# Optimization experiments

Measured on AMD Instinct MI355X. Metric: run time of the kernel, lower is better.

Reference implementation:

```python
import jax, jax.numpy as jnp
import numpy as np

N_NODES, N_EDGES, N_GRAPHS = 200000, 600000, 4000
IN_DIM, EDGE_DIM, HIDDEN, DEPTH = 25, 11, 128, 4
BN_EPS = 1e-5

def lrelu(x):
    return jnp.where(x > 0, x, 0.1 * x)

def setup_inputs() -> dict:
    key = jax.random.key(0)
    ks = jax.random.split(key, 8)
    x = jax.random.normal(ks[0], (N_NODES, IN_DIM), jnp.float32)
    edge_index = jax.random.randint(ks[1], (2, N_EDGES), 0, N_NODES, jnp.int32)
    edge_attr = jax.random.normal(ks[2], (N_EDGES, EDGE_DIM), jnp.float32)
    batch = jnp.sort(jax.random.randint(ks[3], (N_NODES,), 0, N_GRAPHS, jnp.int32))
    def init_w(k, shape, fan_in):
        return jax.random.normal(k, shape, jnp.float32) * np.float32(1.0 / np.sqrt(fan_in))
    W_in = init_w(ks[4], (IN_DIM, HIDDEN), IN_DIM)
    b_in = jnp.zeros((HIDDEN,), jnp.float32)
    W_msg = init_w(ks[5], (DEPTH, HIDDEN + EDGE_DIM, HIDDEN), HIDDEN + EDGE_DIM)
    b_msg = jnp.zeros((DEPTH, HIDDEN), jnp.float32)
    W_up = init_w(ks[6], (DEPTH, 2 * HIDDEN, HIDDEN), 2 * HIDDEN)
    b_up = jnp.zeros((DEPTH, HIDDEN), jnp.float32)
    gamma = jnp.ones((DEPTH, HIDDEN), jnp.float32)
    beta = jnp.zeros((DEPTH, HIDDEN), jnp.float32)
    return dict(x=x, edge_index=edge_index, edge_attr=edge_attr, batch=batch,
                W_in=W_in, b_in=b_in, W_msg=W_msg, b_msg=b_msg,
                W_up=W_up, b_up=b_up, gamma=gamma, beta=beta)

def reference(x, edge_index, edge_attr, batch, W_in, b_in, W_msg, b_msg, W_up, b_up, gamma, beta):
    N = x.shape[0]
    src, dst = edge_index[0], edge_index[1]  # PyG: x_j = x[src], aggregate at dst
    h = lrelu(x @ W_in + b_in)  # input_proj + leaky_relu(0.1)
    depth = W_msg.shape[0]
    for i in range(depth):
        # message: leaky_relu(Linear(cat[x_j, edge_attr]))
        msg = lrelu(jnp.concatenate([h[src], edge_attr], axis=-1) @ W_msg[i] + b_msg[i])
        aggr = jax.ops.segment_sum(msg, dst, num_segments=N)  # scatter-add
        # update: leaky_relu(Linear(cat[aggr, x]))
        out = lrelu(jnp.concatenate([aggr, h], axis=-1) @ W_up[i] + b_up[i])
        out = jax.nn.relu(out)
        # BatchNorm over node dim (training-mode batch statistics)
        mu = out.mean(axis=0)
        var = out.var(axis=0)
        h = gamma[i] * (out - mu) * jax.lax.rsqrt(var + BN_EPS) + beta[i]
        # dropout is identity at eval
    cnt = jax.ops.segment_sum(jnp.ones((N,), h.dtype), batch, num_segments=N_GRAPHS)
    summed = jax.ops.segment_sum(h, batch, num_segments=N_GRAPHS)
    return summed / jnp.maximum(cnt, 1.0)[:, None]  # global_mean_pool -> [G, H]
```

## Files before the change

kernel.cpp:

```cpp
#include <hip/hip_runtime.h>

#define N_NODES  200000
#define N_EDGES  600000
#define N_GRAPHS 4000
#define IN_DIM   25
#define EDGE_DIM 11
#define HIDDEN   128
#define DEPTH    4
#define BN_EPS   1e-5f

#define UB   32
#define NBLK (N_NODES / UB)
#define NEBLK (N_EDGES / 64)
#define CHUNK  256
#define NCHUNK ((N_NODES + CHUNK - 1) / CHUNK)

typedef unsigned short ushortT;
typedef __attribute__((ext_vector_type(8))) short short8v;
typedef __attribute__((ext_vector_type(4))) float float4v;

__device__ __forceinline__ float lrelu(float v) { return v > 0.f ? v : 0.1f * v; }

__device__ __forceinline__ ushortT f2bf(float f) {
    unsigned u = __builtin_bit_cast(unsigned, f);
    u = (u + 0x7fffu + ((u >> 16) & 1u)) >> 16;
    return (ushortT)u;
}
__device__ __forceinline__ float bf2f(ushortT h) {
    unsigned u = ((unsigned)h) << 16;
    return __builtin_bit_cast(float, u);
}

__global__ void k_hist(const int* __restrict__ ei, int* __restrict__ cnt)
{
    const int e = blockIdx.x * 256 + threadIdx.x;
    if (e < N_EDGES) atomicAdd(&cnt[ei[N_EDGES + e]], 1);
}

__global__ __launch_bounds__(256) void k_chunk_sum(const int* __restrict__ cnt,
                                                   int* __restrict__ bsum)
{
    const int t = threadIdx.x;
    const int i = blockIdx.x * CHUNK + t;
    int v = (i < N_NODES) ? cnt[i] : 0;
    #pragma unroll
    for (int off = 32; off > 0; off >>= 1) v += __shfl_down(v, off);
    __shared__ int ws[4];
    if ((t & 63) == 0) ws[t >> 6] = v;
    __syncthreads();
    if (t == 0) bsum[blockIdx.x] = ws[0] + ws[1] + ws[2] + ws[3];
}

__global__ __launch_bounds__(1024) void k_scan_bsums(const int* __restrict__ bsum,
                                                     int* __restrict__ bscan)
{
    __shared__ int s[1024];
    const int t = threadIdx.x;
    const int v = (t < NCHUNK) ? bsum[t] : 0;
    s[t] = v; __syncthreads();
    for (int off = 1; off < 1024; off <<= 1) {
        const int x = (t >= off) ? s[t - off] : 0;
        __syncthreads();
        s[t] += x;
        __syncthreads();
    }
    if (t < NCHUNK) bscan[t] = s[t] - v;
}

__global__ __launch_bounds__(256) void k_chunk_scan(const int* __restrict__ cnt,
                                                    const int* __restrict__ bscan,
                                                    int* __restrict__ off_work)
{
    __shared__ int s[CHUNK];
    const int b = blockIdx.x, t = threadIdx.x;
    const int i = b * CHUNK + t;
    const int v = (i < N_NODES) ? cnt[i] : 0;
    s[t] = v; __syncthreads();
    for (int off = 1; off < CHUNK; off <<= 1) {
        const int x = (t >= off) ? s[t - off] : 0;
        __syncthreads();
        s[t] += x;
        __syncthreads();
    }
    if (i < N_NODES) off_work[i] = bscan[b] + s[t] - v;
}

__global__ void k_scatter(const int* __restrict__ ei, int* __restrict__ off_work,
                          int* __restrict__ srcS, int* __restrict__ dstS,
                          int* __restrict__ perm)
{
    const int e = blockIdx.x * 256 + threadIdx.x;
    if (e < N_EDGES) {
        const int d = ei[N_EDGES + e];
        const int pos = atomicAdd(&off_work[d], 1);
        srcS[pos] = ei[e];
        dstS[pos] = d;
        perm[pos] = e;
    }
}

__global__ void k_flag_ends(const int* __restrict__ dstS, int* __restrict__ flag)
{
    const int i = blockIdx.x * 256 + threadIdx.x;
    if (i < NEBLK * 8) {
        const int b = i >> 3, p = i & 7;
        const int pp = (p >> 1) * 16 + ((p & 1) ? 15 : 0);
        flag[dstS[b * 64 + pp]] = 1;
    }
}

__global__ void k_flag_zdeg(const int* __restrict__ ecnt, int* __restrict__ flag)
{
    const int n = blockIdx.x * 256 + threadIdx.x;
    if (n < N_NODES && ecnt[n] == 0) flag[n] = 1;
}

__global__ void k_compact(const int* __restrict__ flag, int* __restrict__ zlist,
                          int* __restrict__ zcount)
{
    const int n = blockIdx.x * 256 + threadIdx.x;
    if (n < N_NODES && flag[n]) zlist[atomicAdd(zcount, 1)] = n;
}

__global__ __launch_bounds__(256) void k_zero_rows(const int* __restrict__ zlist,
                                                   const int* __restrict__ zcount,
                                                   float* __restrict__ aggr)
{
    const int total = zcount[0] * 32;
    const float4 z = {0.f, 0.f, 0.f, 0.f};
    for (int i = blockIdx.x * 256 + threadIdx.x; i < total; i += gridDim.x * 256) {
        const int row = zlist[i >> 5], q = i & 31;
        reinterpret_cast<float4*>(aggr)[(size_t)row * 32 + q] = z;
    }
}

__global__ __launch_bounds__(256) void k_prep_ea(const float* __restrict__ ea,
                                                 const int* __restrict__ perm,
                                                 ushortT* __restrict__ ea16)
{
    const size_t i = (size_t)blockIdx.x * 256 + threadIdx.x;
    if (i >= (size_t)N_EDGES * 16) return;
    const int e = (int)(i >> 4), c = (int)(i & 15);
    const int pe = perm[e];
    ea16[i] = (c < EDGE_DIM) ? f2bf(ea[(size_t)pe * EDGE_DIM + c]) : (ushortT)0;
}

__global__ __launch_bounds__(256) void k_fold(const float* __restrict__ Wm,
                                              const float* __restrict__ bm,
                                              const float* __restrict__ Wu,
                                              const float* __restrict__ bu,
                                              const float* __restrict__ scale,
                                              const float* __restrict__ shift,
                                              ushortT* __restrict__ WmF,
                                              float*   __restrict__ bmF,
                                              ushortT* __restrict__ WuF,
                                              float*   __restrict__ buF)
{
    const int b = blockIdx.x, t = threadIdx.x;
    if (b < 80) {
        const int i = b * 256 + t;
        const int j = i & 7, lane = (i >> 3) & 63, tile = i >> 9;
        const int ct = tile & 7, kt = tile >> 3;
        const int k = kt * 32 + ((lane >> 4) << 3) + j;
        const int c = ct * 16 + (lane & 15);
        float v = (k < HIDDEN + EDGE_DIM) ? Wm[k * HIDDEN + c] : 0.f;
        if (k < HIDDEN) v *= scale[k];
        WmF[i] = f2bf(v);
    } else if (b < 208) {
        const int i = (b - 80) * 256 + t;
        const int j = i & 7, lane = (i >> 3) & 63, tile = i >> 9;
        const int ct = tile & 7, kt = tile >> 3;
        const int k = kt * 32 + ((lane >> 4) << 3) + j;
        const int c = ct * 16 + (lane & 15);
        float v = Wu[k * HIDDEN + c];
        if (k >= HIDDEN) v *= scale[k - HIDDEN];
        WuF[i] = f2bf(v);
    } else if (b == 208) {
        if (t < HIDDEN) {
            float acc = bm[t];
            for (int k = 0; k < HIDDEN; ++k) acc += shift[k] * Wm[k * HIDDEN + t];
            bmF[t] = acc;
        }
    } else {
        if (t < HIDDEN) {
            float acc = bu[t];
            for (int k = 0; k < HIDDEN; ++k) acc += shift[k] * Wu[(HIDDEN + k) * HIDDEN + t];
            buF[t] = acc;
        }
    }
}

__global__ void k_init_affine(float* __restrict__ scale, float* __restrict__ shift)
{
    const int t = threadIdx.x;
    scale[t] = 1.f;
    shift[t] = 0.f;
}

__global__ __launch_bounds__(128) void k_input_proj(const float* __restrict__ x,
                                                    const float* __restrict__ W,
                                                    const float* __restrict__ b,
                                                    ushortT* __restrict__ h16)
{
    const int t  = threadIdx.x;
    const int n0 = blockIdx.x * 8;
    __shared__ float sW[IN_DIM * HIDDEN];
    __shared__ float sx[8][IN_DIM];
    for (int i = t; i < IN_DIM * HIDDEN; i += 128) sW[i] = W[i];
    for (int i = t; i < 8 * IN_DIM; i += 128) {
        int n = i / IN_DIM, k = i % IN_DIM;
        sx[n][k] = x[(size_t)(n0 + n) * IN_DIM + k];
    }
    __syncthreads();
    const float bt = b[t];
    for (int n = 0; n < 8; ++n) {
        float acc = bt;
        #pragma unroll
        for (int k = 0; k < IN_DIM; ++k) acc += sx[n][k] * sW[k * HIDDEN + t];
        h16[(size_t)(n0 + n) * HIDDEN + t] = f2bf(lrelu(acc));
    }
}

__global__ __launch_bounds__(256) void k_edge_mfma(const ushortT* __restrict__ h16,
                                                   const int*     __restrict__ srcS,
                                                   const int*     __restrict__ dstS,
                                                   const ushortT* __restrict__ ea16,
                                                   const ushortT* __restrict__ Wf,
                                                   const float*   __restrict__ bmsg,
                                                   float*         __restrict__ aggr)
{
    const int t    = threadIdx.x;
    const int wave = t >> 6, lane = t & 63;
    const int e0   = blockIdx.x * 64;

    __shared__ __align__(16) unsigned char smem[64 * 168 * 2];
    ushortT (*sA)[168]   = reinterpret_cast<ushortT (*)[168]>(smem);
    float   (*sMsg)[132] = reinterpret_cast<float (*)[132]>(smem);
    __shared__ int sSrc[64];
    __shared__ int sDst[64];

    const int ct0 = wave * 2;
    short8v B[5][2];
    const short8v* wp = reinterpret_cast<const short8v*>(Wf);
    #pragma unroll
    for (int kt = 0; kt < 5; ++kt) {
        B[kt][0] = wp[(size_t)(kt * 8 + ct0) * 64 + lane];
        B[kt][1] = wp[(size_t)(kt * 8 + ct0 + 1) * 64 + lane];
    }

    if (t < 64) { sSrc[t] = srcS[e0 + t]; sDst[t] = dstS[e0 + t]; }
    __syncthreads();

    for (int i = t; i < 64 * 16; i += 256) {
        const int e = i >> 4, q = i & 15;
        const uint4 v = reinterpret_cast<const uint4*>(h16)[(size_t)sSrc[e] * 16 + q];
        *reinterpret_cast<uint4*>(&sA[e][q * 8]) = v;
    }
    for (int i = t; i < 64 * 2; i += 256) {
        const int e = i >> 1, q = i & 1;
        const uint4 v = reinterpret_cast<const uint4*>(ea16)[((size_t)(e0 + e)) * 2 + q];
        *reinterpret_cast<uint4*>(&sA[e][128 + q * 8]) = v;
    }
    if (t < 128) {
        const int e = t >> 1, q = t & 1;
        const uint4 z = {0u, 0u, 0u, 0u};
        *reinterpret_cast<uint4*>(&sA[e][144 + q * 8]) = z;
    }
    __syncthreads();

    float4v acc[4][2];
    #pragma unroll
    for (int m = 0; m < 4; ++m) { acc[m][0] = (float4v)(0.f); acc[m][1] = (float4v)(0.f); }

    const int kOff = (lane >> 4) * 8;
    #pragma unroll
    for (int m = 0; m < 4; ++m) {
        const int row = m * 16 + (lane & 15);
        #pragma unroll
        for (int kt = 0; kt < 5; ++kt) {
            const short8v a = *reinterpret_cast<const short8v*>(&sA[row][kt * 32 + kOff]);
            acc[m][0] = __builtin_amdgcn_mfma_f32_16x16x32_bf16(a, B[kt][0], acc[m][0], 0, 0, 0);
            acc[m][1] = __builtin_amdgcn_mfma_f32_16x16x32_bf16(a, B[kt][1], acc[m][1], 0, 0, 0);
        }
    }
    __syncthreads();

    const int col = lane & 15;
    const int r0  = (lane >> 4) * 4;
    const int grp = t >> 7;
    const int c   = t & 127;

    #pragma unroll
    for (int phase = 0; phase < 2; ++phase) {
        #pragma unroll
        for (int mm = 0; mm < 2; ++mm) {
            const int m = phase * 2 + mm;
            #pragma unroll
            for (int cc = 0; cc < 2; ++cc) {
                const int ccol = (ct0 + cc) * 16 + col;
                const float bt = bmsg[ccol];
                #pragma unroll
                for (int j = 0; j < 4; ++j) {
                    sMsg[mm * 16 + r0 + j][ccol] = lrelu(acc[m][cc][j] + bt);
                }
            }
        }
        __syncthreads();
        const int base = phase * 32 + grp * 16;
        float a = 0.f;
        int cur = sDst[base];
        bool atStart = true;
        for (int i = 0; i < 16; ++i) {
            const int e = base + i;
            const int d = sDst[e];
            if (d != cur) {
                if (atStart) atomicAdd(&aggr[(size_t)cur * HIDDEN + c], a);
                else         aggr[(size_t)cur * HIDDEN + c] = a;
                atStart = false; cur = d; a = 0.f;
            }
            a += sMsg[e - phase * 32][c];
        }
        atomicAdd(&aggr[(size_t)cur * HIDDEN + c], a);
        __syncthreads();
    }
}

__global__ __launch_bounds__(512) void k_update_mfma(const float*   __restrict__ aggr,
                                                     const ushortT* __restrict__ h16,
                                                     const ushortT* __restrict__ Wf,
                                                     const float*   __restrict__ bup,
                                                     ushortT*       __restrict__ hout,
                                                     float*         __restrict__ p_sum,
                                                     float*         __restrict__ p_sumsq)
{
    const int t    = threadIdx.x;
    const int wave = t >> 6, lane = t & 63;
    const int n0   = blockIdx.x * UB;

    __shared__ __align__(16) ushortT sA[UB][264];
    __shared__ __align__(16) ushortT sLo[UB][136];

    const int ct = wave;
    short8v Bh[8];
    const short8v* wp = reinterpret_cast<const short8v*>(Wf);
    #pragma unroll
    for (int kt = 0; kt < 8; ++kt) Bh[kt] = wp[(size_t)(kt * 8 + ct) * 64 + lane];

    for (int i = t; i < UB * 32; i += 512) {
        const int n = i >> 5, q = i & 31;
        const float4 v = reinterpret_cast<const float4*>(aggr)[(size_t)(n0 + n) * 32 + q];
        union { ushortT s[4]; uint2 u; } hi, lo;
        #pragma unroll
        for (int j = 0; j < 4; ++j) {
            const float f = (&v.x)[j];
            const ushortT hb = f2bf(f);
            hi.s[j] = hb;
            lo.s[j] = f2bf(f - bf2f(hb));
        }
        *reinterpret_cast<uint2*>(&sA[n][q * 4])  = hi.u;
        *reinterpret_cast<uint2*>(&sLo[n][q * 4]) = lo.u;
    }
    for (int i = t; i < UB * 16; i += 512) {
        const int n = i >> 4, q = i & 15;
        const uint4 v = reinterpret_cast<const uint4*>(h16)[(size_t)(n0 + n) * 16 + q];
        *reinterpret_cast<uint4*>(&sA[n][128 + q * 8]) = v;
    }
    __syncthreads();

    float4v acc[2];
    acc[0] = (float4v)(0.f); acc[1] = (float4v)(0.f);

    const int kOff = (lane >> 4) * 8;
    #pragma unroll
    for (int m = 0; m < 2; ++m) {
        const int row = m * 16 + (lane & 15);
        #pragma unroll
        for (int kt = 0; kt < 8; ++kt) {
            const short8v a = *reinterpret_cast<const short8v*>(&sA[row][kt * 32 + kOff]);
            acc[m] = __builtin_amdgcn_mfma_f32_16x16x32_bf16(a, Bh[kt], acc[m], 0, 0, 0);
        }
        #pragma unroll
        for (int kt = 0; kt < 4; ++kt) {
            const short8v a = *reinterpret_cast<const short8v*>(&sLo[row][kt * 32 + kOff]);
            acc[m] = __builtin_amdgcn_mfma_f32_16x16x32_bf16(a, Bh[kt], acc[m], 0, 0, 0);
        }
    }

    const int col  = lane & 15;
    const int r0   = (lane >> 4) * 4;
    const int ccol = ct * 16 + col;
    const float bt = bup[ccol];
    float s = 0.f, q = 0.f;
    #pragma unroll
    for (int m = 0; m < 2; ++m) {
        #pragma unroll
        for (int j = 0; j < 4; ++j) {
            const float v = fmaxf(acc[m][j] + bt, 0.f);
            s += v; q += v * v;
            hout[(size_t)(n0 + m * 16 + r0 + j) * HIDDEN + ccol] = f2bf(v);
        }
    }
    s += __shfl_xor(s, 16); s += __shfl_xor(s, 32);
    q += __shfl_xor(q, 16); q += __shfl_xor(q, 32);
    if (lane < 16) {
        p_sum  [(size_t)blockIdx.x * HIDDEN + ccol] = s;
        p_sumsq[(size_t)blockIdx.x * HIDDEN + ccol] = q;
    }
}

__global__ __launch_bounds__(256) void k_bn_reduce(const float* __restrict__ p_sum,
                                                   const float* __restrict__ p_sumsq,
                                                   const float* __restrict__ gamma,
                                                   const float* __restrict__ beta,
                                                   float* __restrict__ scale,
                                                   float* __restrict__ shift)
{
    const int c = blockIdx.x, t = threadIdx.x;
    float s = 0.f, q = 0.f;
    for (int i = t; i < NBLK; i += 256) {
        s += p_sum  [(size_t)i * HIDDEN + c];
        q += p_sumsq[(size_t)i * HIDDEN + c];
    }
    #pragma unroll
    for (int off = 32; off > 0; off >>= 1) {
        s += __shfl_down(s, off);
        q += __shfl_down(q, off);
    }
    __shared__ float ls[4], lq[4];
    const int w = t >> 6;
    if ((t & 63) == 0) { ls[w] = s; lq[w] = q; }
    __syncthreads();
    if (t == 0) {
        s = ls[0] + ls[1] + ls[2] + ls[3];
        q = lq[0] + lq[1] + lq[2] + lq[3];
        const float mu  = s * (1.f / N_NODES);
        const float var = q * (1.f / N_NODES) - mu * mu;
        const float sc  = gamma[c] * rsqrtf(var + BN_EPS);
        scale[c] = sc;
        shift[c] = beta[c] - mu * sc;
    }
}

__global__ void k_pool_cnt(const int* __restrict__ batch, float* __restrict__ cnt)
{
    const int n = blockIdx.x * 256 + threadIdx.x;
    if (n < N_NODES) atomicAdd(&cnt[batch[n]], 1.0f);
}

__global__ __launch_bounds__(128) void k_pool_sum(const ushortT* __restrict__ h16,
                                                  const int* __restrict__ batch,
                                                  const float* __restrict__ scale,
                                                  const float* __restrict__ shift,
                                                  float* __restrict__ pool)
{
    const int t  = threadIdx.x;
    const int n0 = blockIdx.x * 16;
    __shared__ int sb[16];
    if (t < 16) sb[t] = batch[n0 + t];
    __syncthreads();
    const float sc = scale[t], sh = shift[t];
    int g = sb[0];
    float acc = 0.f;
    for (int j = 0; j < 16; ++j) {
        const float v = sc * bf2f(h16[(size_t)(n0 + j) * HIDDEN + t]) + sh;
        if (sb[j] != g) {
            atomicAdd(&pool[(size_t)g * HIDDEN + t], acc);
            g = sb[j];
            acc = v;
        } else {
            acc += v;
        }
    }
    atomicAdd(&pool[(size_t)g * HIDDEN + t], acc);
}

__global__ void k_pool_div(const float* __restrict__ pool,
                           const float* __restrict__ cnt,
                           float* __restrict__ out)
{
    const int i = blockIdx.x * 256 + threadIdx.x;
    if (i < N_GRAPHS * HIDDEN) {
        const int g = i >> 7;
        out[i] = pool[i] / fmaxf(cnt[g], 1.0f);
    }
}

extern "C" void kernel_launch(void* const* d_in, const int* in_sizes, int n_in,
                              void* d_out, int out_size, void* d_ws, size_t ws_size,
                              hipStream_t stream)
{
    const float* x     = (const float*)d_in[0];
    const int*   ei    = (const int*)  d_in[1];
    const float* ea    = (const float*)d_in[2];
    const int*   batch = (const int*)  d_in[3];
    const float* W_in  = (const float*)d_in[4];
    const float* b_in  = (const float*)d_in[5];
    const float* W_msg = (const float*)d_in[6];
    const float* b_msg = (const float*)d_in[7];
    const float* W_up  = (const float*)d_in[8];
    const float* b_up  = (const float*)d_in[9];
    const float* gamma = (const float*)d_in[10];
    const float* beta  = (const float*)d_in[11];
    float* out = (float*)d_out;

    float*   aggr  = (float*)d_ws;
    ushortT* hA    = (ushortT*)(aggr + (size_t)N_NODES * HIDDEN);
    ushortT* hB    = hA + (size_t)N_NODES * HIDDEN;
    ushortT* ea16  = hB + (size_t)N_NODES * HIDDEN;
    ushortT* wmsgfA = ea16 + (size_t)N_EDGES * 16;
    ushortT* wupfA  = wmsgfA + 20480;
    float*   biasM  = (float*)(wupfA + 32768);
    float*   biasU  = biasM + HIDDEN;
    float*   bn_scale = biasU + HIDDEN;
    float*   bn_shift = bn_scale + HIDDEN;
    float*   pool     = bn_shift + HIDDEN;
    float*   cnt      = pool + (size_t)N_GRAPHS * HIDDEN;
    float*   p_sum    = cnt + N_GRAPHS;
    float*   p_sumsq  = p_sum + (size_t)HIDDEN * NBLK;
    int*     ecnt     = (int*)(p_sumsq + (size_t)HIDDEN * NBLK);
    int*     off_work = ecnt + N_NODES;
    int*     bsum     = off_work + N_NODES;
    int*     bscan    = bsum + 1024;
    int*     srcS     = bscan + 1024;
    int*     dstS     = srcS + N_EDGES;
    int*     perm     = dstS + N_EDGES;
    int*     flag     = perm + N_EDGES;
    int*     zlist    = flag + N_NODES;
    int*     zcount   = zlist + N_NODES;

    hipMemsetAsync(ecnt, 0, N_NODES * sizeof(int), stream);
    hipMemsetAsync(flag, 0, N_NODES * sizeof(int), stream);
    hipMemsetAsync(zcount, 0, sizeof(int), stream);
    k_hist<<<(N_EDGES + 255) / 256, 256, 0, stream>>>(ei, ecnt);
    k_chunk_sum<<<NCHUNK, 256, 0, stream>>>(ecnt, bsum);
    k_scan_bsums<<<1, 1024, 0, stream>>>(bsum, bscan);
    k_chunk_scan<<<NCHUNK, 256, 0, stream>>>(ecnt, bscan, off_work);
    k_scatter<<<(N_EDGES + 255) / 256, 256, 0, stream>>>(ei, off_work, srcS, dstS, perm);
    k_flag_ends<<<(NEBLK * 8 + 255) / 256, 256, 0, stream>>>(dstS, flag);
    k_flag_zdeg<<<(N_NODES + 255) / 256, 256, 0, stream>>>(ecnt, flag);
    k_compact<<<(N_NODES + 255) / 256, 256, 0, stream>>>(flag, zlist, zcount);

    k_prep_ea<<<(N_EDGES * 16 + 255) / 256, 256, 0, stream>>>(ea, perm, ea16);
    k_input_proj<<<N_NODES / 8, 128, 0, stream>>>(x, W_in, b_in, hA);
    k_init_affine<<<1, 128, 0, stream>>>(bn_scale, bn_shift);

    ushortT* hcur = hA;
    ushortT* hnext = hB;
    for (int d = 0; d < DEPTH; ++d) {
        k_fold<<<210, 256, 0, stream>>>(
            W_msg + (size_t)d * (HIDDEN + EDGE_DIM) * HIDDEN, b_msg + (size_t)d * HIDDEN,
            W_up + (size_t)d * 2 * HIDDEN * HIDDEN, b_up + (size_t)d * HIDDEN,
            bn_scale, bn_shift, wmsgfA, biasM, wupfA, biasU);
        k_zero_rows<<<1024, 256, 0, stream>>>(zlist, zcount, aggr);
        k_edge_mfma<<<N_EDGES / 64, 256, 0, stream>>>(
            hcur, srcS, dstS, ea16, wmsgfA, biasM, aggr);
        k_update_mfma<<<N_NODES / UB, 512, 0, stream>>>(
            aggr, hcur, wupfA, biasU, hnext, p_sum, p_sumsq);
        k_bn_reduce<<<HIDDEN, 256, 0, stream>>>(p_sum, p_sumsq,
                                                gamma + (size_t)d * HIDDEN,
                                                beta + (size_t)d * HIDDEN,
                                                bn_scale, bn_shift);
        ushortT* tmp = hcur; hcur = hnext; hnext = tmp;
    }

    hipMemsetAsync(pool, 0, ((size_t)N_GRAPHS * HIDDEN + N_GRAPHS) * sizeof(float), stream);
    k_pool_cnt<<<(N_NODES + 255) / 256, 256, 0, stream>>>(batch, cnt);
    k_pool_sum<<<N_NODES / 16, 128, 0, stream>>>(hcur, batch, bn_scale, bn_shift, pool);
    k_pool_div<<<(N_GRAPHS * HIDDEN + 255) / 256, 256, 0, stream>>>(pool, cnt, out);
}
```

Baseline: 927.6 us.

## Enlarge edge and update tiles and fuse aggregate zeroing into weight fold

The edge kernel now takes 128 edges per block with 512 threads. Each wave owns one 16-column tile and loops over eight row tiles, so each block's weight fragments are reused across twice as many edges. Edges are padded to a multiple of 128 with a dummy destination row, and the list of rows that need zeroing now covers that dummy row. The update kernel handles 64 nodes per block instead of 32. The separate zero-rows launch is merged into the fold kernel as extra blocks, removing one launch per layer. Larger blocks and more accumulators raise register and LDS use, which may lower occupancy.

```diff
diff --git a/kernel.cpp b/kernel.cpp
--- a/kernel.cpp
+++ b/kernel.cpp
@@ -9,9 +9,10 @@
 #define DEPTH    4
 #define BN_EPS   1e-5f
 
-#define UB   32
+#define UB   64
 #define NBLK (N_NODES / UB)
-#define NEBLK (N_EDGES / 64)
+#define EB   128
+#define NEBLK ((N_EDGES + EB - 1) / EB)
 #define CHUNK  256
 #define NCHUNK ((N_NODES + CHUNK - 1) / CHUNK)
 
@@ -99,13 +100,21 @@
     }
 }
 
+__global__ void k_pad_edges(int* __restrict__ srcS, int* __restrict__ dstS,
+                            ushortT* __restrict__ ea16)
+{
+    const int t = threadIdx.x;
+    if (t < 64) { srcS[N_EDGES + t] = 0; dstS[N_EDGES + t] = N_NODES; }
+    ea16[(size_t)N_EDGES * 16 + t] = 0;
+}
+
 __global__ void k_flag_ends(const int* __restrict__ dstS, int* __restrict__ flag)
 {
     const int i = blockIdx.x * 256 + threadIdx.x;
-    if (i < NEBLK * 8) {
-        const int b = i >> 3, p = i & 7;
+    if (i < NEBLK * 16) {
+        const int b = i >> 4, p = i & 15;
         const int pp = (p >> 1) * 16 + ((p & 1) ? 15 : 0);
-        flag[dstS[b * 64 + pp]] = 1;
+        flag[dstS[b * EB + pp]] = 1;
     }
 }
 
@@ -119,19 +128,7 @@
                           int* __restrict__ zcount)
 {
     const int n = blockIdx.x * 256 + threadIdx.x;
-    if (n < N_NODES && flag[n]) zlist[atomicAdd(zcount, 1)] = n;
-}
-
-__global__ __launch_bounds__(256) void k_zero_rows(const int* __restrict__ zlist,
-                                                   const int* __restrict__ zcount,
-                                                   float* __restrict__ aggr)
-{
-    const int total = zcount[0] * 32;
-    const float4 z = {0.f, 0.f, 0.f, 0.f};
-    for (int i = blockIdx.x * 256 + threadIdx.x; i < total; i += gridDim.x * 256) {
-        const int row = zlist[i >> 5], q = i & 31;
-        reinterpret_cast<float4*>(aggr)[(size_t)row * 32 + q] = z;
-    }
+    if (n < N_NODES + 1 && flag[n]) zlist[atomicAdd(zcount, 1)] = n;
 }
 
 __global__ __launch_bounds__(256) void k_prep_ea(const float* __restrict__ ea,
@@ -154,7 +151,10 @@
                                               ushortT* __restrict__ WmF,
                                               float*   __restrict__ bmF,
                                               ushortT* __restrict__ WuF,
-                                              float*   __restrict__ buF)
+                                              float*   __restrict__ buF,
+                                              const int* __restrict__ zlist,
+                                              const int* __restrict__ zcount,
+                                              float* __restrict__ aggr)
 {
     const int b = blockIdx.x, t = threadIdx.x;
     if (b < 80) {
@@ -181,11 +181,18 @@
             for (int k = 0; k < HIDDEN; ++k) acc += shift[k] * Wm[k * HIDDEN + t];
             bmF[t] = acc;
         }
-    } else {
+    } else if (b == 209) {
         if (t < HIDDEN) {
             float acc = bu[t];
             for (int k = 0; k < HIDDEN; ++k) acc += shift[k] * Wu[(HIDDEN + k) * HIDDEN + t];
             buF[t] = acc;
+        }
+    } else {
+        const int total = zcount[0] * 32;
+        const float4 z = {0.f, 0.f, 0.f, 0.f};
+        for (int i = (b - 210) * 256 + t; i < total; i += 256 * 256) {
+            const int row = zlist[i >> 5], q = i & 31;
+            reinterpret_cast<float4*>(aggr)[(size_t)row * 32 + q] = z;
         }
     }
 }
@@ -221,7 +228,7 @@
     }
 }
 
-__global__ __launch_bounds__(256) void k_edge_mfma(const ushortT* __restrict__ h16,
+__global__ __launch_bounds__(512) void k_edge_mfma(const ushortT* __restrict__ h16,
                                                    const int*     __restrict__ srcS,
                                                    const int*     __restrict__ dstS,
                                                    const ushortT* __restrict__ ea16,
@@ -231,82 +238,71 @@
 {
     const int t    = threadIdx.x;
     const int wave = t >> 6, lane = t & 63;
-    const int e0   = blockIdx.x * 64;
-
-    __shared__ __align__(16) unsigned char smem[64 * 168 * 2];
+    const int e0   = blockIdx.x * EB;
+
+    __shared__ __align__(16) unsigned char smem[EB * 168 * 2];
     ushortT (*sA)[168]   = reinterpret_cast<ushortT (*)[168]>(smem);
     float   (*sMsg)[132] = reinterpret_cast<float (*)[132]>(smem);
-    __shared__ int sSrc[64];
-    __shared__ int sDst[64];
-
-    const int ct0 = wave * 2;
-    short8v B[5][2];
+    __shared__ int sSrc[EB];
+    __shared__ int sDst[EB];
+
+    const int ct = wave;
+    short8v B[5];
     const short8v* wp = reinterpret_cast<const short8v*>(Wf);
     #pragma unroll
-    for (int kt = 0; kt < 5; ++kt) {
-        B[kt][0] = wp[(size_t)(kt * 8 + ct0) * 64 + lane];
-        B[kt][1] = wp[(size_t)(kt * 8 + ct0 + 1) * 64 + lane];
-    }
-
-    if (t < 64) { sSrc[t] = srcS[e0 + t]; sDst[t] = dstS[e0 + t]; }
-    __syncthreads();
-
-    for (int i = t; i < 64 * 16; i += 256) {
+    for (int kt = 0; kt < 5; ++kt) B[kt] = wp[(size_t)(kt * 8 + ct) * 64 + lane];
+
+    if (t < EB) { sSrc[t] = srcS[e0 + t]; sDst[t] = dstS[e0 + t]; }
+    __syncthreads();
+
+    for (int i = t; i < EB * 16; i += 512) {
         const int e = i >> 4, q = i & 15;
         const uint4 v = reinterpret_cast<const uint4*>(h16)[(size_t)sSrc[e] * 16 + q];
         *reinterpret_cast<uint4*>(&sA[e][q * 8]) = v;
     }
-    for (int i = t; i < 64 * 2; i += 256) {
-        const int e = i >> 1, q = i & 1;
+    if (t < EB * 2) {
+        const int e = t >> 1, q = t & 1;
         const uint4 v = reinterpret_cast<const uint4*>(ea16)[((size_t)(e0 + e)) * 2 + q];
         *reinterpret_cast<uint4*>(&sA[e][128 + q * 8]) = v;
-    }
-    if (t < 128) {
-        const int e = t >> 1, q = t & 1;
         const uint4 z = {0u, 0u, 0u, 0u};
         *reinterpret_cast<uint4*>(&sA[e][144 + q * 8]) = z;
     }
     __syncthreads();
 
-    float4v acc[4][2];
-    #pragma unroll
-    for (int m = 0; m < 4; ++m) { acc[m][0] = (float4v)(0.f); acc[m][1] = (float4v)(0.f); }
+    float4v acc[8];
+    #pragma unroll
+    for (int m = 0; m < 8; ++m) acc[m] = (float4v)(0.f);
 
     const int kOff = (lane >> 4) * 8;
     #pragma unroll
-    for (int m = 0; m < 4; ++m) {
+    for (int m = 0; m < 8; ++m) {
         const int row = m * 16 + (lane & 15);
         #pragma unroll
         for (int kt = 0; kt < 5; ++kt) {
             const short8v a = *reinterpret_cast<const short8v*>(&sA[row][kt * 32 + kOff]);
-            acc[m][0] = __builtin_amdgcn_mfma_f32_16x16x32_bf16(a, B[kt][0], acc[m][0], 0, 0, 0);
-            acc[m][1] = __builtin_amdgcn_mfma_f32_16x16x32_bf16(a, B[kt][1], acc[m][1], 0, 0, 0);
+            acc[m] = __builtin_amdgcn_mfma_f32_16x16x32_bf16(a, B[kt], acc[m], 0, 0, 0);
         }
     }
     __syncthreads();
 
     const int col = lane & 15;
     const int r0  = (lane >> 4) * 4;
-    const int grp = t >> 7;
+    const float bt = bmsg[ct * 16 + col];
     const int c   = t & 127;
-
-    #pragma unroll
-    for (int phase = 0; phase < 2; ++phase) {
-        #pragma unroll
-        for (int mm = 0; mm < 2; ++mm) {
-            const int m = phase * 2 + mm;
+    const int g   = t >> 7;
+
+    #pragma unroll
+    for (int p = 0; p < 2; ++p) {
+        #pragma unroll
+        for (int mm = 0; mm < 4; ++mm) {
+            const int m = p * 4 + mm;
             #pragma unroll
-            for (int cc = 0; cc < 2; ++cc) {
-                const int ccol = (ct0 + cc) * 16 + col;
-                const float bt = bmsg[ccol];
-                #pragma unroll
-                for (int j = 0; j < 4; ++j) {
-                    sMsg[mm * 16 + r0 + j][ccol] = lrelu(acc[m][cc][j] + bt);
-                }
+            for (int j = 0; j < 4; ++j) {
+                sMsg[mm * 16 + r0 + j][ct * 16 + col] = lrelu(acc[m][j] + bt);
             }
         }
         __syncthreads();
-        const int base = phase * 32 + grp * 16;
+        const int base = p * 64 + g * 16;
         float a = 0.f;
         int cur = sDst[base];
         bool atStart = true;
@@ -318,7 +314,7 @@
                 else         aggr[(size_t)cur * HIDDEN + c] = a;
                 atStart = false; cur = d; a = 0.f;
             }
-            a += sMsg[e - phase * 32][c];
+            a += sMsg[e - p * 64][c];
         }
         atomicAdd(&aggr[(size_t)cur * HIDDEN + c], a);
         __syncthreads();
@@ -367,12 +363,13 @@
     }
     __syncthreads();
 
-    float4v acc[2];
-    acc[0] = (float4v)(0.f); acc[1] = (float4v)(0.f);
+    float4v acc[4];
+    #pragma unroll
+    for (int m = 0; m < 4; ++m) acc[m] = (float4v)(0.f);
 
     const int kOff = (lane >> 4) * 8;
     #pragma unroll
-    for (int m = 0; m < 2; ++m) {
+    for (int m = 0; m < 4; ++m) {
         const int row = m * 16 + (lane & 15);
         #pragma unroll
         for (int kt = 0; kt < 8; ++kt) {
@@ -392,7 +389,7 @@
     const float bt = bup[ccol];
     float s = 0.f, q = 0.f;
     #pragma unroll
-    for (int m = 0; m < 2; ++m) {
+    for (int m = 0; m < 4; ++m) {
         #pragma unroll
         for (int j = 0; j < 4; ++j) {
             const float v = fmaxf(acc[m][j] + bt, 0.f);
@@ -504,10 +501,10 @@
     float* out = (float*)d_out;
 
     float*   aggr  = (float*)d_ws;
-    ushortT* hA    = (ushortT*)(aggr + (size_t)N_NODES * HIDDEN);
+    ushortT* hA    = (ushortT*)(aggr + (size_t)(N_NODES + 1) * HIDDEN);
     ushortT* hB    = hA + (size_t)N_NODES * HIDDEN;
     ushortT* ea16  = hB + (size_t)N_NODES * HIDDEN;
-    ushortT* wmsgfA = ea16 + (size_t)N_EDGES * 16;
+    ushortT* wmsgfA = ea16 + (size_t)(N_EDGES + 64) * 16;
     ushortT* wupfA  = wmsgfA + 20480;
     float*   biasM  = (float*)(wupfA + 32768);
     float*   biasU  = biasM + HIDDEN;
@@ -522,23 +519,24 @@
     int*     bsum     = off_work + N_NODES;
     int*     bscan    = bsum + 1024;
     int*     srcS     = bscan + 1024;
-    int*     dstS     = srcS + N_EDGES;
-    int*     perm     = dstS + N_EDGES;
+    int*     dstS     = srcS + (N_EDGES + 64);
+    int*     perm     = dstS + (N_EDGES + 64);
     int*     flag     = perm + N_EDGES;
-    int*     zlist    = flag + N_NODES;
-    int*     zcount   = zlist + N_NODES;
+    int*     zlist    = flag + (N_NODES + 1);
+    int*     zcount   = zlist + (N_NODES + 1);
 
     hipMemsetAsync(ecnt, 0, N_NODES * sizeof(int), stream);
-    hipMemsetAsync(flag, 0, N_NODES * sizeof(int), stream);
+    hipMemsetAsync(flag, 0, (N_NODES + 1) * sizeof(int), stream);
     hipMemsetAsync(zcount, 0, sizeof(int), stream);
     k_hist<<<(N_EDGES + 255) / 256, 256, 0, stream>>>(ei, ecnt);
     k_chunk_sum<<<NCHUNK, 256, 0, stream>>>(ecnt, bsum);
     k_scan_bsums<<<1, 1024, 0, stream>>>(bsum, bscan);
     k_chunk_scan<<<NCHUNK, 256, 0, stream>>>(ecnt, bscan, off_work);
     k_scatter<<<(N_EDGES + 255) / 256, 256, 0, stream>>>(ei, off_work, srcS, dstS, perm);
-    k_flag_ends<<<(NEBLK * 8 + 255) / 256, 256, 0, stream>>>(dstS, flag);
+    k_pad_edges<<<1, 1024, 0, stream>>>(srcS, dstS, ea16);
+    k_flag_ends<<<(NEBLK * 16 + 255) / 256, 256, 0, stream>>>(dstS, flag);
     k_flag_zdeg<<<(N_NODES + 255) / 256, 256, 0, stream>>>(ecnt, flag);
-    k_compact<<<(N_NODES + 255) / 256, 256, 0, stream>>>(flag, zlist, zcount);
+    k_compact<<<(N_NODES + 256) / 256, 256, 0, stream>>>(flag, zlist, zcount);
 
     k_prep_ea<<<(N_EDGES * 16 + 255) / 256, 256, 0, stream>>>(ea, perm, ea16);
     k_input_proj<<<N_NODES / 8, 128, 0, stream>>>(x, W_in, b_in, hA);
@@ -547,12 +545,12 @@
     ushortT* hcur = hA;
     ushortT* hnext = hB;
     for (int d = 0; d < DEPTH; ++d) {
-        k_fold<<<210, 256, 0, stream>>>(
+        k_fold<<<466, 256, 0, stream>>>(
             W_msg + (size_t)d * (HIDDEN + EDGE_DIM) * HIDDEN, b_msg + (size_t)d * HIDDEN,
             W_up + (size_t)d * 2 * HIDDEN * HIDDEN, b_up + (size_t)d * HIDDEN,
-            bn_scale, bn_shift, wmsgfA, biasM, wupfA, biasU);
-        k_zero_rows<<<1024, 256, 0, stream>>>(zlist, zcount, aggr);
-        k_edge_mfma<<<N_EDGES / 64, 256, 0, stream>>>(
+            bn_scale, bn_shift, wmsgfA, biasM, wupfA, biasU,
+            zlist, zcount, aggr);
+        k_edge_mfma<<<NEBLK, 512, 0, stream>>>(
             hcur, srcS, dstS, ea16, wmsgfA, biasM, aggr);
         k_update_mfma<<<N_NODES / UB, 512, 0, stream>>>(
             aggr, hcur, wupfA, biasU, hnext, p_sum, p_sumsq);
```

After: 851.4 us. 1.09x faster.
